# Kernel tuning notes

Hardware: AMD Instinct MI355X
Metric: run time of the kernel (lower is better)

Reference implementation:

```python
import jax, jax.numpy as jnp
import numpy as np

N = 20000      # nodes
E = 320000     # edges (avg degree 16)
IN, HID, OUT, H = 128, 32, 32, 8
NEG_SLOPE = 0.2


def _gat_conv(x, src, dst, W, al, ar, b):
    """One DGL-style GATConv. x: [N, F_in], W: [F_in, H*D], al/ar: [H, D], b: [H*D].
    Returns [N, H, D]."""
    n = x.shape[0]
    Hh, D = al.shape
    feat = (x @ W).reshape(n, Hh, D)                      # [N,H,D]
    el = jnp.sum(feat * al[None], axis=-1)                # [N,H]
    er = jnp.sum(feat * ar[None], axis=-1)                # [N,H]
    e = jax.nn.leaky_relu(el[src] + er[dst], NEG_SLOPE)   # [E,H]
    # edge softmax over incoming edges of each dst node (stable)
    emax = jax.ops.segment_max(e, dst, num_segments=n)    # [N,H]
    ee = jnp.exp(e - emax[dst])                           # [E,H]
    denom = jax.ops.segment_sum(ee, dst, num_segments=n)  # [N,H]
    alpha = ee / denom[dst]                               # [E,H]
    msg = feat[src] * alpha[:, :, None]                   # [E,H,D] gather+weight
    out = jax.ops.segment_sum(msg, dst, num_segments=n)   # [N,H,D] scatter-add
    return out + b.reshape(1, Hh, D)


def setup_inputs() -> dict:
    key = jax.random.key(0)
    ks = jax.random.split(key, 11)
    return {
        "x":   jax.random.normal(ks[0], (N, IN), dtype=jnp.float32),
        "src": jax.random.randint(ks[1], (E,), 0, N, dtype=jnp.int32),
        "dst": jax.random.randint(ks[2], (E,), 0, N, dtype=jnp.int32),
        "W1":  jax.random.normal(ks[3], (IN, H * HID), dtype=jnp.float32) * 0.1,
        "al1": jax.random.normal(ks[4], (H, HID), dtype=jnp.float32) * 0.1,
        "ar1": jax.random.normal(ks[5], (H, HID), dtype=jnp.float32) * 0.1,
        "b1":  jnp.zeros((H * HID,), dtype=jnp.float32),
        "W2":  jax.random.normal(ks[6], (HID, H * OUT), dtype=jnp.float32) * 0.1,
        "al2": jax.random.normal(ks[7], (H, OUT), dtype=jnp.float32) * 0.1,
        "ar2": jax.random.normal(ks[8], (H, OUT), dtype=jnp.float32) * 0.1,
        "b2":  jnp.zeros((H * OUT,), dtype=jnp.float32),
    }


def reference(x, src, dst, W1, al1, ar1, b1, W2, al2, ar2, b2):
    h = _gat_conv(x, src, dst, W1, al1, ar1, b1)          # [N,H,HID]
    h = jnp.mean(jax.nn.relu(h), axis=1)                  # [N,HID]
    h = _gat_conv(h, src, dst, W2, al2, ar2, b2)          # [N,H,OUT]
    return jnp.mean(h, axis=1)                            # [N,OUT]
```

## Files before the change

kernel.cpp:

```cpp
#include <hip/hip_runtime.h>
#include <hip/hip_bf16.h>

#define N_NODES 20000
#define N_EDGES 320000
#define F_IN    128
#define F_HID   32
#define NHEAD   8
#define FDIM    256
#define CAP     96

typedef __hip_bfloat16 bf16;
typedef __attribute__((ext_vector_type(8))) short short8;
typedef __attribute__((ext_vector_type(4))) float f32x4;

__device__ __forceinline__ unsigned short f2bf_rne(float f){
  unsigned u = __float_as_uint(f);
  unsigned r = u + 0x7FFFu + ((u >> 16) & 1u);
  return (unsigned short)(r >> 16);
}
__device__ __forceinline__ float bf2f(unsigned short s){
  return __uint_as_float((unsigned)s << 16);
}

__global__ void zero_kernel(int* __restrict__ p, int n){
  int i = blockIdx.x*256 + threadIdx.x;
  if (i < n) p[i] = 0;
}

__global__ void fill_bucket_kernel(const int* __restrict__ src, const int* __restrict__ dst,
                                   int* __restrict__ cnt, int* __restrict__ bucket, int e){
  int i = blockIdx.x*256 + threadIdx.x;
  if (i < e){
    int d = dst[i];
    int p = atomicAdd(&cnt[d], 1);
    if (p < CAP) bucket[(size_t)d*CAP + p] = src[i];
  }
}

__global__ void split_kernel(const float* __restrict__ in,
                             unsigned short* __restrict__ hi,
                             unsigned short* __restrict__ lo, int n4){
  int i = blockIdx.x*256 + threadIdx.x;
  if (i < n4){
    float4 v = ((const float4*)in)[i];
    ushort4 h, l;
    h.x = f2bf_rne(v.x); l.x = f2bf_rne(v.x - bf2f(h.x));
    h.y = f2bf_rne(v.y); l.y = f2bf_rne(v.y - bf2f(h.y));
    h.z = f2bf_rne(v.z); l.z = f2bf_rne(v.z - bf2f(h.z));
    h.w = f2bf_rne(v.w); l.w = f2bf_rne(v.w - bf2f(h.w));
    ((ushort4*)hi)[i] = h;
    ((ushort4*)lo)[i] = l;
  }
}

template<int K>
__global__ void splitT_kernel(const float* __restrict__ W,
                              unsigned short* __restrict__ hi,
                              unsigned short* __restrict__ lo){
  int i = blockIdx.x*256 + threadIdx.x;
  int n = i / K, k = i - n*K;
  float v = W[(size_t)k*FDIM + n];
  unsigned short hs = f2bf_rne(v);
  hi[i] = hs;
  lo[i] = f2bf_rne(v - bf2f(hs));
}

template<int K>
__global__ __launch_bounds__(256) void gemm_mfma_kernel(
    const unsigned short* __restrict__ Xhi, const unsigned short* __restrict__ Xlo,
    const unsigned short* __restrict__ Wthi, const unsigned short* __restrict__ Wtlo,
    const float* __restrict__ al, const float* __restrict__ ar,
    unsigned short* __restrict__ feat, float* __restrict__ el, float* __restrict__ er)
{
  const int tid  = threadIdx.x;
  const int wv   = tid >> 6;
  const int lane = tid & 63;
  const int quad = lane >> 4;
  const int l16  = lane & 15;
  const int m0   = blockIdx.x * 16;
  constexpr int NC = K / 32;

  short8 Ah[NC], Al_[NC];
  const size_t arow = (size_t)(m0 + l16) * K;
  #pragma unroll
  for (int c = 0; c < NC; c++){
    Ah[c]  = *(const short8*)(Xhi + arow + c*32 + quad*8);
    Al_[c] = *(const short8*)(Xlo + arow + c*32 + quad*8);
  }

  float elp[8], erp[8];
  #pragma unroll
  for (int j = 0; j < 8; j++){ elp[j] = 0.f; erp[j] = 0.f; }

  #pragma unroll
  for (int t = 0; t < 4; t++){
    const int nc = wv*64 + t*16;
    const size_t brow = (size_t)(nc + l16) * K;
    f32x4 acc = {0.f, 0.f, 0.f, 0.f};
    #pragma unroll
    for (int c = 0; c < NC; c++){
      short8 Bh = *(const short8*)(Wthi + brow + c*32 + quad*8);
      short8 Bl = *(const short8*)(Wtlo + brow + c*32 + quad*8);
      acc = __builtin_amdgcn_mfma_f32_16x16x32_bf16(Ah[c],  Bh, acc, 0, 0, 0);
      acc = __builtin_amdgcn_mfma_f32_16x16x32_bf16(Ah[c],  Bl, acc, 0, 0, 0);
      acc = __builtin_amdgcn_mfma_f32_16x16x32_bf16(Al_[c], Bh, acc, 0, 0, 0);
    }
    const float alv = al[nc + l16];
    const float arv = ar[nc + l16];
    const int hl = t >> 1;
    #pragma unroll
    for (int r = 0; r < 4; r++){
      float v = acc[r];
      feat[(size_t)(m0 + quad*4 + r)*FDIM + nc + l16] = f2bf_rne(v);
      elp[r*2 + hl] = fmaf(v, alv, elp[r*2 + hl]);
      erp[r*2 + hl] = fmaf(v, arv, erp[r*2 + hl]);
    }
  }

  #pragma unroll
  for (int off = 1; off <= 8; off <<= 1){
    #pragma unroll
    for (int j = 0; j < 8; j++){
      elp[j] += __shfl_xor(elp[j], off);
      erp[j] += __shfl_xor(erp[j], off);
    }
  }
  __shared__ float el_lds[16][8], er_lds[16][8];
  if (l16 == 0){
    #pragma unroll
    for (int r = 0; r < 4; r++){
      #pragma unroll
      for (int hl = 0; hl < 2; hl++){
        el_lds[quad*4 + r][wv*2 + hl] = elp[r*2 + hl];
        er_lds[quad*4 + r][wv*2 + hl] = erp[r*2 + hl];
      }
    }
  }
  __syncthreads();
  if (tid < 128){
    int row = tid >> 3, h = tid & 7;
    el[(size_t)(m0 + row)*NHEAD + h] = el_lds[row][h];
    er[(size_t)(m0 + row)*NHEAD + h] = er_lds[row][h];
  }
}

template<int RELU_MEAN>
__global__ __launch_bounds__(256) void edge_agg_kernel(
    const bf16* __restrict__ feat, const float* __restrict__ el,
    const float* __restrict__ er, const int* __restrict__ cnt,
    const int* __restrict__ bucket, const float* __restrict__ bias,
    float* __restrict__ outp)
{
  const int tid  = threadIdx.x;
  const int wv   = tid >> 6;
  const int lane = tid & 63;
  const int n    = blockIdx.x*4 + wv;

  __shared__ float t_all[4][CAP*9];
  __shared__ int   s_all[4][CAP];
  __shared__ float sum_all[4][NHEAD];
  __shared__ float v_all[4][256];
  float* t_w = t_all[wv];
  int*   s_w = s_all[wv];

  int C = cnt[n];
  if (C > CAP) C = CAP;

  const float4* er4 = (const float4*)(er + (size_t)n*NHEAD);
  float4 era = er4[0], erb = er4[1];
  const float erv[8] = {era.x, era.y, era.z, era.w, erb.x, erb.y, erb.z, erb.w};

  for (int e = lane; e < C; e += 64){
    const int sidx = bucket[(size_t)n*CAP + e];
    s_w[e] = sidx;
    const float4* e4 = (const float4*)(el + (size_t)sidx*NHEAD);
    float4 a = e4[0], bq = e4[1];
    float ev[8] = {a.x, a.y, a.z, a.w, bq.x, bq.y, bq.z, bq.w};
    #pragma unroll
    for (int hh = 0; hh < 8; hh++){
      float v = ev[hh] + erv[hh];
      t_w[e*9 + hh] = (v > 0.f) ? v : 0.2f*v;
    }
  }
  {
    const int h = lane >> 3, d = lane & 7;
    float lm = -INFINITY;
    for (int e = d; e < C; e += 8) lm = fmaxf(lm, t_w[e*9 + h]);
    #pragma unroll
    for (int off = 4; off >= 1; off >>= 1) lm = fmaxf(lm, __shfl_xor(lm, off));
    float ls = 0.f;
    for (int e = d; e < C; e += 8){
      float ex = __expf(t_w[e*9 + h] - lm);
      t_w[e*9 + h] = ex;
      ls += ex;
    }
    #pragma unroll
    for (int off = 4; off >= 1; off >>= 1) ls += __shfl_xor(ls, off);
    if (d == 0) sum_all[wv][h] = ls;
  }

  const int sub = lane >> 5;
  const int l   = lane & 31;
  const int hB  = l >> 2;
  float acc[8] = {0,0,0,0,0,0,0,0};
  for (int e = sub; e < C; e += 2){
    const int sidx = s_w[e];
    const float4 fv = *(const float4*)(feat + (size_t)sidx*FDIM + (l << 3));
    const float w = t_w[e*9 + hB];
    const unsigned* u = (const unsigned*)&fv;
    #pragma unroll
    for (int j = 0; j < 4; j++){
      float flo = __uint_as_float(u[j] << 16);
      float fhi = __uint_as_float(u[j] & 0xFFFF0000u);
      acc[2*j]   = fmaf(w, flo, acc[2*j]);
      acc[2*j+1] = fmaf(w, fhi, acc[2*j+1]);
    }
  }
  #pragma unroll
  for (int j = 0; j < 8; j++) acc[j] += __shfl_xor(acc[j], 32);

  if (lane < 32){
    const float s = sum_all[wv][l >> 2];
    const float4* b4 = (const float4*)(bias + (l << 3));
    float4 ba = b4[0], bb = b4[1];
    float bv[8] = {ba.x, ba.y, ba.z, ba.w, bb.x, bb.y, bb.z, bb.w};
    float v[8];
    #pragma unroll
    for (int j = 0; j < 8; j++){
      float val = (C > 0) ? (acc[j] / s) : 0.f;
      val += bv[j];
      if (RELU_MEAN) val = fmaxf(val, 0.f);
      v[j] = val;
    }
    float4* v4 = (float4*)&v_all[wv][l << 3];
    v4[0] = make_float4(v[0], v[1], v[2], v[3]);
    v4[1] = make_float4(v[4], v[5], v[6], v[7]);
  }
  if (lane < 32){
    float sum = 0.f;
    #pragma unroll
    for (int hh = 0; hh < 8; hh++) sum += v_all[wv][hh*32 + lane];
    sum *= 0.125f;
    outp[(size_t)n*32 + lane] = sum;
  }
}

extern "C" void kernel_launch(void* const* d_in, const int* in_sizes, int n_in,
                              void* d_out, int out_size, void* d_ws, size_t ws_size,
                              hipStream_t stream)
{
  const float* x   = (const float*)d_in[0];
  const int*   src = (const int*)  d_in[1];
  const int*   dst = (const int*)  d_in[2];
  const float* W1  = (const float*)d_in[3];
  const float* al1 = (const float*)d_in[4];
  const float* ar1 = (const float*)d_in[5];
  const float* b1  = (const float*)d_in[6];
  const float* W2  = (const float*)d_in[7];
  const float* al2 = (const float*)d_in[8];
  const float* ar2 = (const float*)d_in[9];
  const float* b2  = (const float*)d_in[10];
  (void)in_sizes; (void)n_in; (void)out_size; (void)ws_size;

  size_t o = 0;
  char* base = (char*)d_ws;
  auto take = [&](size_t bytes) -> char* {
    char* p = base + o;
    o += (bytes + 255) & ~(size_t)255;
    return p;
  };
  unsigned short* feat  = (unsigned short*)take((size_t)N_NODES*FDIM*2);
  float* el     = (float*)take((size_t)N_NODES*NHEAD*4);
  float* er     = (float*)take((size_t)N_NODES*NHEAD*4);
  float* hbuf   = (float*)take((size_t)N_NODES*F_HID*4);
  int*   cnt    = (int*)  take((size_t)N_NODES*4);
  int*   bucket = (int*)  take((size_t)N_NODES*CAP*4);
  unsigned short* Xhi  = (unsigned short*)take((size_t)N_NODES*F_IN*2);
  unsigned short* Xlo  = (unsigned short*)take((size_t)N_NODES*F_IN*2);
  unsigned short* Hhi  = (unsigned short*)take((size_t)N_NODES*F_HID*2);
  unsigned short* Hlo  = (unsigned short*)take((size_t)N_NODES*F_HID*2);
  unsigned short* W1th = (unsigned short*)take((size_t)FDIM*F_IN*2);
  unsigned short* W1tl = (unsigned short*)take((size_t)FDIM*F_IN*2);
  unsigned short* W2th = (unsigned short*)take((size_t)FDIM*F_HID*2);
  unsigned short* W2tl = (unsigned short*)take((size_t)FDIM*F_HID*2);

  zero_kernel<<<(N_NODES+255)/256, 256, 0, stream>>>(cnt, N_NODES);
  fill_bucket_kernel<<<(N_EDGES+255)/256, 256, 0, stream>>>(src, dst, cnt, bucket, N_EDGES);
  split_kernel<<<(N_NODES*F_IN/4+255)/256, 256, 0, stream>>>(x, Xhi, Xlo, N_NODES*F_IN/4);
  splitT_kernel<F_IN ><<<(FDIM*F_IN )/256, 256, 0, stream>>>(W1, W1th, W1tl);
  splitT_kernel<F_HID><<<(FDIM*F_HID)/256, 256, 0, stream>>>(W2, W2th, W2tl);

  gemm_mfma_kernel<F_IN><<<N_NODES/16, 256, 0, stream>>>(
      Xhi, Xlo, W1th, W1tl, al1, ar1, feat, el, er);
  edge_agg_kernel<1><<<N_NODES/4, 256, 0, stream>>>(
      (const bf16*)feat, el, er, cnt, bucket, b1, hbuf);

  split_kernel<<<(N_NODES*F_HID/4+255)/256, 256, 0, stream>>>(hbuf, Hhi, Hlo, N_NODES*F_HID/4);
  gemm_mfma_kernel<F_HID><<<N_NODES/16, 256, 0, stream>>>(
      Hhi, Hlo, W2th, W2tl, al2, ar2, feat, el, er);
  edge_agg_kernel<0><<<N_NODES/4, 256, 0, stream>>>(
      (const bf16*)feat, el, er, cnt, bucket, b2, (float*)d_out);
}
```

Baseline: 209.7 us.

## Fuse bf16 hi/lo splitting into GEMM and aggregation kernels, merge weight splits

The layer-1 GEMM now converts fp32 x to bf16 hi/lo pairs in registers instead of relying on a separate split kernel and its intermediate buffers. The layer-1 aggregation writes its hidden output directly as hi/lo bf16, which removes the second split kernel and the fp32 hidden buffer. The two weight-transpose split kernels become one launch, and the zero kernel is replaced by hipMemsetAsync. This cuts kernel launches and intermediate global traffic. In exchange the GEMM does a little more conversion arithmetic per block, and each block loads x rows in fp32, which is twice the bytes of the bf16 form.

```diff
diff --git a/kernel.cpp b/kernel.cpp
--- a/kernel.cpp
+++ b/kernel.cpp
@@ -22,11 +22,6 @@
   return __uint_as_float((unsigned)s << 16);
 }
 
-__global__ void zero_kernel(int* __restrict__ p, int n){
-  int i = blockIdx.x*256 + threadIdx.x;
-  if (i < n) p[i] = 0;
-}
-
 __global__ void fill_bucket_kernel(const int* __restrict__ src, const int* __restrict__ dst,
                                    int* __restrict__ cnt, int* __restrict__ bucket, int e){
   int i = blockIdx.x*256 + threadIdx.x;
@@ -37,37 +32,30 @@
   }
 }
 
-__global__ void split_kernel(const float* __restrict__ in,
-                             unsigned short* __restrict__ hi,
-                             unsigned short* __restrict__ lo, int n4){
+__global__ void splitT_both_kernel(const float* __restrict__ W1, const float* __restrict__ W2,
+                                   unsigned short* __restrict__ h1, unsigned short* __restrict__ l1,
+                                   unsigned short* __restrict__ h2, unsigned short* __restrict__ l2){
   int i = blockIdx.x*256 + threadIdx.x;
-  if (i < n4){
-    float4 v = ((const float4*)in)[i];
-    ushort4 h, l;
-    h.x = f2bf_rne(v.x); l.x = f2bf_rne(v.x - bf2f(h.x));
-    h.y = f2bf_rne(v.y); l.y = f2bf_rne(v.y - bf2f(h.y));
-    h.z = f2bf_rne(v.z); l.z = f2bf_rne(v.z - bf2f(h.z));
-    h.w = f2bf_rne(v.w); l.w = f2bf_rne(v.w - bf2f(h.w));
-    ((ushort4*)hi)[i] = h;
-    ((ushort4*)lo)[i] = l;
-  }
-}
-
-template<int K>
-__global__ void splitT_kernel(const float* __restrict__ W,
-                              unsigned short* __restrict__ hi,
-                              unsigned short* __restrict__ lo){
-  int i = blockIdx.x*256 + threadIdx.x;
-  int n = i / K, k = i - n*K;
-  float v = W[(size_t)k*FDIM + n];
-  unsigned short hs = f2bf_rne(v);
-  hi[i] = hs;
-  lo[i] = f2bf_rne(v - bf2f(hs));
-}
-
-template<int K>
+  const int n1 = FDIM*F_IN;
+  if (i < n1){
+    int n = i / F_IN, k = i - n*F_IN;
+    float v = W1[(size_t)k*FDIM + n];
+    unsigned short hs = f2bf_rne(v);
+    h1[i] = hs;
+    l1[i] = f2bf_rne(v - bf2f(hs));
+  } else {
+    int j = i - n1;
+    int n = j / F_HID, k = j - n*F_HID;
+    float v = W2[(size_t)k*FDIM + n];
+    unsigned short hs = f2bf_rne(v);
+    h2[j] = hs;
+    l2[j] = f2bf_rne(v - bf2f(hs));
+  }
+}
+
+template<int K, int XSPLIT>
 __global__ __launch_bounds__(256) void gemm_mfma_kernel(
-    const unsigned short* __restrict__ Xhi, const unsigned short* __restrict__ Xlo,
+    const void* __restrict__ Xa, const void* __restrict__ Xb,
     const unsigned short* __restrict__ Wthi, const unsigned short* __restrict__ Wtlo,
     const float* __restrict__ al, const float* __restrict__ ar,
     unsigned short* __restrict__ feat, float* __restrict__ el, float* __restrict__ er)
@@ -81,11 +69,27 @@
   constexpr int NC = K / 32;
 
   short8 Ah[NC], Al_[NC];
-  const size_t arow = (size_t)(m0 + l16) * K;
-  #pragma unroll
-  for (int c = 0; c < NC; c++){
-    Ah[c]  = *(const short8*)(Xhi + arow + c*32 + quad*8);
-    Al_[c] = *(const short8*)(Xlo + arow + c*32 + quad*8);
+  if (XSPLIT){
+    const float* xrow = (const float*)Xa + (size_t)(m0 + l16)*K;
+    #pragma unroll
+    for (int c = 0; c < NC; c++){
+      float4 a0 = *(const float4*)(xrow + c*32 + quad*8);
+      float4 a1 = *(const float4*)(xrow + c*32 + quad*8 + 4);
+      const float vs[8] = {a0.x,a0.y,a0.z,a0.w,a1.x,a1.y,a1.z,a1.w};
+      #pragma unroll
+      for (int j = 0; j < 8; j++){
+        unsigned short hs = f2bf_rne(vs[j]);
+        Ah[c][j]  = (short)hs;
+        Al_[c][j] = (short)f2bf_rne(vs[j] - bf2f(hs));
+      }
+    }
+  } else {
+    const size_t arow = (size_t)(m0 + l16) * K;
+    #pragma unroll
+    for (int c = 0; c < NC; c++){
+      Ah[c]  = *(const short8*)((const unsigned short*)Xa + arow + c*32 + quad*8);
+      Al_[c] = *(const short8*)((const unsigned short*)Xb + arow + c*32 + quad*8);
+    }
   }
 
   float elp[8], erp[8];
@@ -144,12 +148,13 @@
   }
 }
 
-template<int RELU_MEAN>
+template<int SPLIT_OUT>
 __global__ __launch_bounds__(256) void edge_agg_kernel(
     const bf16* __restrict__ feat, const float* __restrict__ el,
     const float* __restrict__ er, const int* __restrict__ cnt,
     const int* __restrict__ bucket, const float* __restrict__ bias,
-    float* __restrict__ outp)
+    float* __restrict__ outp,
+    unsigned short* __restrict__ ohi, unsigned short* __restrict__ olo)
 {
   const int tid  = threadIdx.x;
   const int wv   = tid >> 6;
@@ -229,7 +234,7 @@
     for (int j = 0; j < 8; j++){
       float val = (C > 0) ? (acc[j] / s) : 0.f;
       val += bv[j];
-      if (RELU_MEAN) val = fmaxf(val, 0.f);
+      if (SPLIT_OUT) val = fmaxf(val, 0.f);
       v[j] = val;
     }
     float4* v4 = (float4*)&v_all[wv][l << 3];
@@ -241,7 +246,13 @@
     #pragma unroll
     for (int hh = 0; hh < 8; hh++) sum += v_all[wv][hh*32 + lane];
     sum *= 0.125f;
-    outp[(size_t)n*32 + lane] = sum;
+    if (SPLIT_OUT){
+      unsigned short hs = f2bf_rne(sum);
+      ohi[(size_t)n*32 + lane] = hs;
+      olo[(size_t)n*32 + lane] = f2bf_rne(sum - bf2f(hs));
+    } else {
+      outp[(size_t)n*32 + lane] = sum;
+    }
   }
 }
 
@@ -272,11 +283,8 @@
   unsigned short* feat  = (unsigned short*)take((size_t)N_NODES*FDIM*2);
   float* el     = (float*)take((size_t)N_NODES*NHEAD*4);
   float* er     = (float*)take((size_t)N_NODES*NHEAD*4);
-  float* hbuf   = (float*)take((size_t)N_NODES*F_HID*4);
   int*   cnt    = (int*)  take((size_t)N_NODES*4);
   int*   bucket = (int*)  take((size_t)N_NODES*CAP*4);
-  unsigned short* Xhi  = (unsigned short*)take((size_t)N_NODES*F_IN*2);
-  unsigned short* Xlo  = (unsigned short*)take((size_t)N_NODES*F_IN*2);
   unsigned short* Hhi  = (unsigned short*)take((size_t)N_NODES*F_HID*2);
   unsigned short* Hlo  = (unsigned short*)take((size_t)N_NODES*F_HID*2);
   unsigned short* W1th = (unsigned short*)take((size_t)FDIM*F_IN*2);
@@ -284,20 +292,18 @@
   unsigned short* W2th = (unsigned short*)take((size_t)FDIM*F_HID*2);
   unsigned short* W2tl = (unsigned short*)take((size_t)FDIM*F_HID*2);
 
-  zero_kernel<<<(N_NODES+255)/256, 256, 0, stream>>>(cnt, N_NODES);
+  hipMemsetAsync(cnt, 0, (size_t)N_NODES*4, stream);
   fill_bucket_kernel<<<(N_EDGES+255)/256, 256, 0, stream>>>(src, dst, cnt, bucket, N_EDGES);
-  split_kernel<<<(N_NODES*F_IN/4+255)/256, 256, 0, stream>>>(x, Xhi, Xlo, N_NODES*F_IN/4);
-  splitT_kernel<F_IN ><<<(FDIM*F_IN )/256, 256, 0, stream>>>(W1, W1th, W1tl);
-  splitT_kernel<F_HID><<<(FDIM*F_HID)/256, 256, 0, stream>>>(W2, W2th, W2tl);
-
-  gemm_mfma_kernel<F_IN><<<N_NODES/16, 256, 0, stream>>>(
-      Xhi, Xlo, W1th, W1tl, al1, ar1, feat, el, er);
+  splitT_both_kernel<<<(FDIM*(F_IN+F_HID))/256, 256, 0, stream>>>(
+      W1, W2, W1th, W1tl, W2th, W2tl);
+
+  gemm_mfma_kernel<F_IN, 1><<<N_NODES/16, 256, 0, stream>>>(
+      x, nullptr, W1th, W1tl, al1, ar1, feat, el, er);
   edge_agg_kernel<1><<<N_NODES/4, 256, 0, stream>>>(
-      (const bf16*)feat, el, er, cnt, bucket, b1, hbuf);
-
-  split_kernel<<<(N_NODES*F_HID/4+255)/256, 256, 0, stream>>>(hbuf, Hhi, Hlo, N_NODES*F_HID/4);
-  gemm_mfma_kernel<F_HID><<<N_NODES/16, 256, 0, stream>>>(
+      (const bf16*)feat, el, er, cnt, bucket, b1, nullptr, Hhi, Hlo);
+
+  gemm_mfma_kernel<F_HID, 0><<<N_NODES/16, 256, 0, stream>>>(
       Hhi, Hlo, W2th, W2tl, al2, ar2, feat, el, er);
   edge_agg_kernel<0><<<N_NODES/4, 256, 0, stream>>>(
-      (const bf16*)feat, el, er, cnt, bucket, b2, (float*)d_out);
-}
+      (const bf16*)feat, el, er, cnt, bucket, b2, (float*)d_out, nullptr, nullptr);
+}
```

Result: faster. 197.8 us (-5.7%).
